# Optimization experiments

Measured on AMD Instinct MI355X. Metric: run time of the kernel, lower is better.

Reference implementation:

```python
import jax, jax.numpy as jnp
import numpy as np

N_NODES = 20000
N_EDGES = 320000
N_GRAPHS = 200
N_LAYERS = 2
TOWERS = 5
F_IN = 75        # divide_input=False -> each tower sees the full 75-dim input
F_OUT = 15       # out_channels // towers = 75 // 5
EDGE_DIM = 50
POST_IN = (4 * 3 + 1) * F_IN  # 4 aggregators * 3 scalers + self = 975
EPS_STD = 1e-5
EPS_BN = 1e-5


def setup_inputs() -> dict:
    key = jax.random.key(0)
    ks = jax.random.split(key, 16)
    x_idx = jax.random.randint(ks[0], (N_NODES,), 0, 10000)
    edge_index = jax.random.randint(ks[1], (2, N_EDGES), 0, N_NODES)
    edge_attr_idx = jax.random.randint(ks[2], (N_EDGES,), 0, 100)
    batch_idx = jnp.sort(jax.random.randint(ks[3], (N_NODES,), 0, N_GRAPHS))

    def g(k, shp, fan):
        return jax.random.normal(k, shp, jnp.float32) * np.float32(1.0 / np.sqrt(fan))

    inp = dict(
        x_idx=x_idx, edge_index=edge_index, edge_attr_idx=edge_attr_idx, batch_idx=batch_idx,
        node_emb=g(ks[4], (10000, F_IN), 1.0),
        edge_emb=g(ks[5], (100, EDGE_DIM), 1.0),
        W_edge=g(ks[6], (N_LAYERS, EDGE_DIM, F_IN), EDGE_DIM),
        b_edge=jnp.zeros((N_LAYERS, F_IN), jnp.float32),
        W_pre=g(ks[7], (N_LAYERS, TOWERS, 3 * F_IN, F_IN), 3 * F_IN),
        b_pre=jnp.zeros((N_LAYERS, TOWERS, F_IN), jnp.float32),
        W_post=g(ks[8], (N_LAYERS, TOWERS, POST_IN, F_OUT), POST_IN),
        b_post=jnp.zeros((N_LAYERS, TOWERS, F_OUT), jnp.float32),
        W_lin=g(ks[9], (N_LAYERS, F_IN, F_IN), F_IN),
        b_lin=jnp.zeros((N_LAYERS, F_IN), jnp.float32),
        bn_gamma=jnp.ones((N_LAYERS, F_IN), jnp.float32),
        bn_beta=jnp.zeros((N_LAYERS, F_IN), jnp.float32),
        W1=g(ks[10], (75, 50), 75), b1=jnp.zeros((50,), jnp.float32),
        W2=g(ks[11], (50, 25), 50), b2=jnp.zeros((25,), jnp.float32),
        W3=g(ks[12], (25, 1), 25), b3=jnp.zeros((1,), jnp.float32),
    )
    return inp


def reference(x_idx, edge_index, edge_attr_idx, batch_idx,
              node_emb, edge_emb, W_edge, b_edge, W_pre, b_pre,
              W_post, b_post, W_lin, b_lin, bn_gamma, bn_beta,
              W1, b1, W2, b2, W3, b3):
    src, dst = edge_index[0], edge_index[1]  # flow source_to_target: aggregate at dst
    x = node_emb[x_idx]                      # [N, 75]
    e_raw = edge_emb[edge_attr_idx]          # [E, 50]

    # in-degree based scalers (PNA); avg log-degree from this graph's degree histogram
    deg = jax.ops.segment_sum(jnp.ones((N_EDGES,), jnp.float32), dst, num_segments=N_NODES)
    avg_log = jnp.mean(jnp.log(deg + 1.0))
    deg_c = jnp.maximum(deg, 1.0)
    amp = (jnp.log(deg_c + 1.0) / avg_log)[:, None, None]
    att = (avg_log / jnp.log(deg_c + 1.0))[:, None, None]
    has_in = (deg > 0.0)[:, None, None]
    inv_deg = (1.0 / deg_c)[:, None, None]

    for l in range(N_LAYERS):
        # edge encoder (shared across towers)
        e = e_raw @ W_edge[l] + b_edge[l]                            # [E, 75]
        # message: since divide_input=False all towers see the same concat input
        h = jnp.concatenate([x[dst], x[src], e], axis=-1)            # [E, 225]
        m = jnp.einsum('ec,tcf->etf', h, W_pre[l]) + b_pre[l]        # [E, T, 75]
        # multi-aggregator reduction at dst
        mean = jax.ops.segment_sum(m, dst, num_segments=N_NODES) * inv_deg
        mean_sq = jax.ops.segment_sum(m * m, dst, num_segments=N_NODES) * inv_deg
        std = jnp.sqrt(jax.nn.relu(mean_sq - mean * mean) + EPS_STD)
        mn = jnp.where(has_in, jax.ops.segment_min(m, dst, num_segments=N_NODES), 0.0)
        mx = jnp.where(has_in, jax.ops.segment_max(m, dst, num_segments=N_NODES), 0.0)
        aggr = jnp.concatenate([mean, mn, mx, std], axis=-1)         # [N, T, 300]
        # degree scalers: identity, amplification, attenuation
        out = jnp.concatenate([aggr, aggr * amp, aggr * att], axis=-1)  # [N, T, 900]
        # update: concat self features, per-tower post MLP, then shared lin
        xt = jnp.broadcast_to(x[:, None, :], (N_NODES, TOWERS, F_IN))
        h2 = jnp.concatenate([xt, out], axis=-1)                     # [N, T, 975]
        y = jnp.einsum('ntc,tcf->ntf', h2, W_post[l]) + b_post[l]    # [N, T, 15]
        y = y.reshape(N_NODES, TOWERS * F_OUT) @ W_lin[l] + b_lin[l] # [N, 75]
        # BatchNorm (training-mode batch stats, biased variance) + ReLU
        mu = jnp.mean(y, axis=0)
        var = jnp.mean((y - mu) ** 2, axis=0)
        y = (y - mu) * jax.lax.rsqrt(var + EPS_BN) * bn_gamma[l] + bn_beta[l]
        x = jax.nn.relu(y)

    pooled = jax.ops.segment_sum(x, batch_idx, num_segments=N_GRAPHS)  # [G, 75]
    h = jax.nn.relu(pooled @ W1 + b1)
    h = jax.nn.relu(h @ W2 + b2)
    return h @ W3 + b3                                               # [G, 1]
```

## Files before the change

kernel.cpp:

```cpp
#include <hip/hip_runtime.h>
#include <hip/hip_bf16.h>
#include <math.h>

#define NN 20000
#define NE 320000
#define NG 200
#define FI 75
#define NT 5
#define FO 15
#define CH 375
#define PI 975

typedef __attribute__((ext_vector_type(8))) short v8s;
typedef __attribute__((ext_vector_type(4))) float v4f;

__device__ __forceinline__ unsigned short f2bfu(float v) {
  __hip_bfloat16 h = __float2bfloat16(v);
  return *reinterpret_cast<unsigned short*>(&h);
}
__device__ __forceinline__ float uif(unsigned u) { return __uint_as_float(u); }

__global__ __launch_bounds__(256) void k_mega1(
    const int* __restrict__ xidx, const float* __restrict__ emb, float* __restrict__ x,
    const int* __restrict__ dstp, int* __restrict__ deg,
    const float* __restrict__ eemb, const float* __restrict__ W_edge,
    const float* __restrict__ b_edge, float* __restrict__ te,
    const float* __restrict__ W_pre, float* __restrict__ WAs,
    const float* __restrict__ W_post, float* __restrict__ V,
    const float* __restrict__ b_post, const float* __restrict__ W_lin,
    const float* __restrict__ b_lin, float* __restrict__ bc) {
  __shared__ float S[FI * 16];
  int b = blockIdx.x, tid = threadIdx.x;
  if (b < 5860) {
    int i = b * 256 + tid;
    if (i < NN * FI) {
      int n = i / FI, f = i - n * FI;
      x[i] = emb[xidx[n] * FI + f];
    }
  } else if (b < 7110) {
    int e = (b - 5860) * 256 + tid;
    if (e < NE) atomicAdd(&deg[dstp[e]], 1);
  } else if (b < 7310) {
    int la = b - 7110;
    int l = la / 100, a = la - l * 100;
    int f = tid;
    if (f < FI) {
      float acc = b_edge[l * FI + f];
      for (int j = 0; j < 50; ++j)
        acc = fmaf(eemb[a * 50 + j], W_edge[(l * 50 + j) * FI + f], acc);
      te[la * FI + f] = acc;
    }
  } else if (b < 7530) {
    int i = (b - 7310) * 256 + tid;
    if (i < 2 * FI * CH) {
      int c = i % CH;
      int k = (i / CH) % FI;
      int l = i / (CH * FI);
      int t = c / FI, f = c - t * FI;
      WAs[i] = W_pre[((size_t)(l * NT + t) * 225 + FI + k) * FI + f];
    }
  } else if (b < 7560) {
    int bid = b - 7530;
    int g = bid % 3;
    int lt = bid / 3;
    for (int idx = tid; idx < FI * 16; idx += 256) {
      int q = idx >> 4, f = idx & 15;
      float v = 0.f;
      if (f < FO) {
        const float* wb = W_post + (size_t)lt * PI * FO;
        int rowb = FI + g * 300 + q;
        v = wb[rowb * FO + f] + wb[(rowb + FI) * FO + f] + wb[(rowb + 2 * FI) * FO + f];
      }
      S[idx] = v;
    }
    __syncthreads();
    for (int idx = tid; idx < FI * 16; idx += 256) {
      int j = idx >> 4, f = idx & 15;
      float acc = 0.f;
      const float* wr = W_pre + ((size_t)lt * 225 + j) * FI;
      for (int q = 0; q < FI; ++q) acc = fmaf(wr[q], S[q * 16 + f], acc);
      V[((size_t)bid * FI + j) * 16 + f] = acc;
    }
  } else {
    int l = b - 7560;
    int g = tid;
    if (g < FI) {
      float acc = b_lin[l * FI + g];
      for (int j = 0; j < FI; ++j)
        acc = fmaf(b_post[l * FI + j], W_lin[(l * FI + j) * FI + g], acc);
      bc[l * 76 + g] = acc;
    }
  }
}

__global__ __launch_bounds__(1024) void k_mega2(
    const int* __restrict__ deg, int* __restrict__ off, int* __restrict__ cur,
    float* __restrict__ avglog,
    const float* __restrict__ te, const float* __restrict__ W_pre,
    const float* __restrict__ b_pre, unsigned short* __restrict__ tm,
    const float* __restrict__ W_post, const float* __restrict__ V,
    unsigned short* __restrict__ Bp,
    const float* __restrict__ WAs, unsigned short* __restrict__ Bxs,
    const float* __restrict__ W_lin, unsigned short* __restrict__ Blin) {
  __shared__ float red[1024];
  int b = blockIdx.x, t = threadIdx.x;
  if (b == 0) {
    int* wsum = (int*)red;
    int base = t * 20;
    int loc[20];
    int s = 0;
#pragma unroll
    for (int j = 0; j < 20; ++j) {
      int i = base + j;
      int v = (i < NN) ? deg[i] : 0;
      loc[j] = s;
      s += v;
    }
    int lane = t & 63, w = t >> 6;
    int inc = s;
    for (int o = 1; o < 64; o <<= 1) {
      int u = __shfl_up(inc, o, 64);
      if (lane >= o) inc += u;
    }
    if (lane == 63) wsum[w] = inc;
    __syncthreads();
    if (t == 0) {
      int a = 0;
#pragma unroll
      for (int k = 0; k < 16; ++k) { int v = wsum[k]; wsum[k] = a; a += v; }
    }
    __syncthreads();
    int tex = wsum[w] + inc - s;
#pragma unroll
    for (int j = 0; j < 20; ++j) {
      int i = base + j;
      if (i < NN) { int e = tex + loc[j]; off[i] = e; cur[i] = e; }
    }
    if (t == 1023) off[NN] = tex + s;
  } else if (b == 1) {
    float s = 0.f;
    for (int i = t; i < NN; i += 1024) s += logf((float)deg[i] + 1.f);
    red[t] = s;
    __syncthreads();
    for (int o = 512; o > 0; o >>= 1) {
      if (t < o) red[t] += red[t + o];
      __syncthreads();
    }
    if (t == 0) avglog[0] = red[0] / (float)NN;
  } else if (b < 77) {
    int idx = (b - 2) * 1024 + t;
    if (idx < 76800) {
      int la = idx / 384, c = idx - la * 384;
      int l = la / 100;
      float acc = 0.f;
      if (c < CH) {
        int tt = c / FI, f = c - tt * FI;
        acc = b_pre[(l * NT + tt) * FI + f];
        const float* ter = te + la * FI;
        for (int k = 0; k < FI; ++k)
          acc = fmaf(ter[k], W_pre[((size_t)(l * NT + tt) * 225 + 150 + k) * FI + f], acc);
      }
      tm[(size_t)la * 384 + c] = f2bfu(acc);
    }
  } else if (b < 302) {
    int i = (b - 77) * 1024 + t;
    if (i < 230400) {
      int j = i & 7;
      int lane = (i >> 3) & 63;
      int rem = i >> 9;
      int kb = rem % 15; rem /= 15;
      int g = rem % 3; rem /= 3;
      int tt = rem % 5;
      int l = rem / 5;
      int k = kb * 32 + (lane >> 4) * 8 + j;
      int f = lane & 15;
      float w = 0.f;
      if (f < FO) {
        int lt = l * NT + tt;
        if (k < 300) {
          int a = k / 75, ch = k - a * 75;
          w = W_post[((size_t)lt * PI + FI + g * 300 + a * 75 + ch) * FO + f];
        } else if (k >= 320 && k < 395) {
          w = V[(((size_t)(lt * 3 + g)) * FI + (k - 320)) * 16 + f];
        } else if (k >= 395 && k < 470 && g == 0) {
          w = W_post[((size_t)lt * PI + (k - 395)) * FO + f];
        }
      }
      Bp[i] = f2bfu(w);
    }
  } else if (b < 374) {
    int i = (b - 302) * 1024 + t;
    if (i < 73728) {
      int j = i & 7;
      int lane = (i >> 3) & 63;
      int rem = i >> 9;
      int nt = rem % 24; rem /= 24;
      int kb = rem % 3;
      int l = rem / 3;
      int k = kb * 32 + (lane >> 4) * 8 + j;
      int n = nt * 16 + (lane & 15);
      float w = 0.f;
      if (k < FI && n < CH) w = WAs[(size_t)l * FI * CH + k * CH + n];
      Bxs[i] = f2bfu(w);
    }
  } else {
    int i = (b - 374) * 1024 + t;
    if (i < 15360) {
      int j = i & 7;
      int lane = (i >> 3) & 63;
      int rem = i >> 9;
      int nt = rem % 5; rem /= 5;
      int kb = rem % 3;
      int l = rem / 3;
      int k = kb * 32 + (lane >> 4) * 8 + j;
      int f = nt * 16 + (lane & 15);
      float w = 0.f;
      if (k < FI && f < FI) w = W_lin[(size_t)l * FI * FI + k * FI + f];
      Blin[i] = f2bfu(w);
    }
  }
}

__global__ __launch_bounds__(256) void k_mega3(
    const int* __restrict__ srcp, const int* __restrict__ dstp,
    const int* __restrict__ attr, int* __restrict__ cur, int2* __restrict__ csr,
    const int* __restrict__ deg, const float* __restrict__ avglog,
    float* __restrict__ amp, float* __restrict__ att, float* __restrict__ inv) {
  int b = blockIdx.x, t = threadIdx.x;
  if (b < 1250) {
    int e = b * 256 + t;
    if (e < NE) {
      int pos = atomicAdd(&cur[dstp[e]], 1);
      csr[pos] = make_int2(srcp[e], attr[e]);
    }
  } else {
    int i = (b - 1250) * 256 + t;
    if (i < NN) {
      float dc = fmaxf((float)deg[i], 1.f);
      float ld = logf(dc + 1.f);
      float av = avglog[0];
      amp[i] = ld / av;
      att[i] = av / ld;
      inv[i] = 1.f / dc;
    }
  }
}

__global__ __launch_bounds__(256) void k_gemm_xs(const float* __restrict__ x,
                                                 const unsigned short* __restrict__ BxsL,
                                                 unsigned short* __restrict__ xsb,
                                                 const int* __restrict__ deg,
                                                 unsigned short* __restrict__ xh,
                                                 float* __restrict__ bnsum) {
  int tid = threadIdx.x;
  if (blockIdx.y == 1) {
    if (blockIdx.x == 0 && tid < 150) bnsum[tid] = 0.f;
    for (int i = blockIdx.x * 256 + tid; i < NN * 160; i += 625 * 256) {
      int r = i / 160, k = i - r * 160;
      float v = 0.f;
      if (k < FI) v = x[(size_t)r * FI + k] * ((deg[r] > 0) ? 1.f : 0.f);
      else if (k < 150) v = x[(size_t)r * FI + k - FI];
      xh[i] = f2bfu(v);
    }
    return;
  }
  __shared__ unsigned short As[32 * 104];
  __shared__ unsigned short Os[32 * 384];
  int m0 = blockIdx.x * 32;
  for (int i = tid; i < 32 * 104; i += 256) {
    int r = i / 104, k = i - r * 104;
    As[i] = (k < FI) ? f2bfu(x[(size_t)(m0 + r) * FI + k]) : 0;
  }
  __syncthreads();
  int lane = tid & 63, w = tid >> 6;
  int m16 = lane & 15, quad = lane >> 4;
  v4f acc0[6], acc1[6];
#pragma unroll
  for (int nt = 0; nt < 6; ++nt) {
    acc0[nt] = {0.f, 0.f, 0.f, 0.f};
    acc1[nt] = {0.f, 0.f, 0.f, 0.f};
  }
  const unsigned short* arow0 = As + m16 * 104 + quad * 8;
  const unsigned short* arow1 = As + (16 + m16) * 104 + quad * 8;
#pragma unroll
  for (int kb = 0; kb < 3; ++kb) {
    v8s a0 = *(const v8s*)(arow0 + kb * 32);
    v8s a1 = *(const v8s*)(arow1 + kb * 32);
#pragma unroll
    for (int nt = 0; nt < 6; ++nt) {
      v8s bf = *(const v8s*)(BxsL + ((size_t)(kb * 24 + w * 6 + nt) * 64 + lane) * 8);
      acc0[nt] = __builtin_amdgcn_mfma_f32_16x16x32_bf16(a0, bf, acc0[nt], 0, 0, 0);
      acc1[nt] = __builtin_amdgcn_mfma_f32_16x16x32_bf16(a1, bf, acc1[nt], 0, 0, 0);
    }
  }
#pragma unroll
  for (int nt = 0; nt < 6; ++nt) {
    int col = w * 96 + nt * 16 + m16;
#pragma unroll
    for (int r = 0; r < 4; ++r) {
      Os[(quad * 4 + r) * 384 + col] = f2bfu(acc0[nt][r]);
      Os[(16 + quad * 4 + r) * 384 + col] = f2bfu(acc1[nt][r]);
    }
  }
  __syncthreads();
  uint4* dst = (uint4*)(xsb + (size_t)m0 * 384);
  const uint4* src = (const uint4*)Os;
  for (int i = tid; i < 1536; i += 256) dst[i] = src[i];
}

__global__ __launch_bounds__(192) void k_aggregate(int n0, int cn,
    const unsigned short* __restrict__ xs, const int2* __restrict__ csr,
    const int* __restrict__ off, const float* __restrict__ inv_deg,
    const unsigned short* __restrict__ tm, unsigned short* __restrict__ aggA) {
  __shared__ unsigned short sm[4 * 1600];
  int tid = threadIdx.x;
  int sub = tid / 48;
  int lane48 = tid - sub * 48;
  int rel0 = blockIdx.x * 4;
  int rel = rel0 + sub;
  for (int idx = tid; idx < 400; idx += 192) {
    int h = idx / 100, pp = idx - h * 100;
    int t = pp / 20, cc = pp - t * 20;
    sm[h * 1600 + t * 320 + 300 + cc] = 0;
  }
  if (rel < cn) {
    int n = n0 + rel;
    int c0 = lane48 * 8;
    int o0 = off[n], o1 = off[n + 1];
    float s[8], q[8], mn[8], mx[8];
#pragma unroll
    for (int j = 0; j < 8; ++j) {
      s[j] = 0.f; q[j] = 0.f; mn[j] = INFINITY; mx[j] = -INFINITY;
    }
    auto proc = [&](uint4 xv, uint4 tv) {
      unsigned xa[4] = {xv.x, xv.y, xv.z, xv.w};
      unsigned ta[4] = {tv.x, tv.y, tv.z, tv.w};
#pragma unroll
      for (int j = 0; j < 4; ++j) {
        float z0 = uif(xa[j] << 16) + uif(ta[j] << 16);
        float z1 = uif(xa[j] & 0xffff0000u) + uif(ta[j] & 0xffff0000u);
        s[2 * j] += z0; q[2 * j] = fmaf(z0, z0, q[2 * j]);
        mn[2 * j] = fminf(mn[2 * j], z0); mx[2 * j] = fmaxf(mx[2 * j], z0);
        s[2 * j + 1] += z1; q[2 * j + 1] = fmaf(z1, z1, q[2 * j + 1]);
        mn[2 * j + 1] = fminf(mn[2 * j + 1], z1); mx[2 * j + 1] = fmaxf(mx[2 * j + 1], z1);
      }
    };
    int i = o0;
    for (; i + 8 <= o1; i += 8) {
      int2 e0 = csr[i], e1 = csr[i + 1], e2 = csr[i + 2], e3 = csr[i + 3];
      int2 e4 = csr[i + 4], e5 = csr[i + 5], e6 = csr[i + 6], e7 = csr[i + 7];
      uint4 x0 = *(const uint4*)(xs + (size_t)e0.x * 384 + c0);
      uint4 t0 = *(const uint4*)(tm + (size_t)e0.y * 384 + c0);
      uint4 x1 = *(const uint4*)(xs + (size_t)e1.x * 384 + c0);
      uint4 t1 = *(const uint4*)(tm + (size_t)e1.y * 384 + c0);
      uint4 x2 = *(const uint4*)(xs + (size_t)e2.x * 384 + c0);
      uint4 t2 = *(const uint4*)(tm + (size_t)e2.y * 384 + c0);
      uint4 x3 = *(const uint4*)(xs + (size_t)e3.x * 384 + c0);
      uint4 t3 = *(const uint4*)(tm + (size_t)e3.y * 384 + c0);
      uint4 x4 = *(const uint4*)(xs + (size_t)e4.x * 384 + c0);
      uint4 t4 = *(const uint4*)(tm + (size_t)e4.y * 384 + c0);
      uint4 x5 = *(const uint4*)(xs + (size_t)e5.x * 384 + c0);
      uint4 t5 = *(const uint4*)(tm + (size_t)e5.y * 384 + c0);
      uint4 x6 = *(const uint4*)(xs + (size_t)e6.x * 384 + c0);
      uint4 t6 = *(const uint4*)(tm + (size_t)e6.y * 384 + c0);
      uint4 x7 = *(const uint4*)(xs + (size_t)e7.x * 384 + c0);
      uint4 t7 = *(const uint4*)(tm + (size_t)e7.y * 384 + c0);
      proc(x0, t0); proc(x1, t1); proc(x2, t2); proc(x3, t3);
      proc(x4, t4); proc(x5, t5); proc(x6, t6); proc(x7, t7);
    }
    for (; i + 2 <= o1; i += 2) {
      int2 e0 = csr[i], e1 = csr[i + 1];
      uint4 x0 = *(const uint4*)(xs + (size_t)e0.x * 384 + c0);
      uint4 t0 = *(const uint4*)(tm + (size_t)e0.y * 384 + c0);
      uint4 x1 = *(const uint4*)(xs + (size_t)e1.x * 384 + c0);
      uint4 t1 = *(const uint4*)(tm + (size_t)e1.y * 384 + c0);
      proc(x0, t0); proc(x1, t1);
    }
    if (i < o1) {
      int2 e0 = csr[i];
      uint4 x0 = *(const uint4*)(xs + (size_t)e0.x * 384 + c0);
      uint4 t0 = *(const uint4*)(tm + (size_t)e0.y * 384 + c0);
      proc(x0, t0);
    }
    float inv = inv_deg[n];
    bool empty = (o1 == o0);
    unsigned short* srow = sm + sub * 1600;
#pragma unroll
    for (int j = 0; j < 8; ++j) {
      int c = c0 + j;
      if (c < CH) {
        float me = s[j] * inv;
        float sd = sqrtf(fmaxf(q[j] * inv - me * me, 0.f) + 1e-5f);
        float mnv = empty ? 0.f : mn[j];
        float mxv = empty ? 0.f : mx[j];
        int t = c / 75, ch = c - t * 75;
        unsigned short* bb = srow + t * 320;
        bb[ch] = f2bfu(me);
        bb[75 + ch] = f2bfu(mnv);
        bb[150 + ch] = f2bfu(mxv);
        bb[225 + ch] = f2bfu(sd);
      }
    }
  }
  __syncthreads();
  int nrow = cn - rel0;
  if (nrow > 4) nrow = 4;
  if (nrow > 0) {
    int nu4 = nrow * 200;
    uint4* dst = (uint4*)(aggA + (size_t)rel0 * 1600);
    const uint4* src = (const uint4*)sm;
    for (int idx = tid; idx < nu4; idx += 192) dst[idx] = src[idx];
  }
}

__global__ __launch_bounds__(320) void k_post2(int n0, int nend,
    const unsigned short* __restrict__ aggA, const unsigned short* __restrict__ xh,
    const unsigned short* __restrict__ Bp, const float* __restrict__ amp,
    const float* __restrict__ att, const unsigned short* __restrict__ BlinL,
    const float* __restrict__ bcL, float* __restrict__ yout,
    float* __restrict__ bnsum) {
  __shared__ unsigned short zs[16 * 96];
  __shared__ float ysum[FI], ysq[FI];
  int tid = threadIdx.x;
  int lane = tid & 63, wv = tid >> 6;
  int m16 = lane & 15, quad = lane >> 4;
  if (tid < FI) { ysum[tid] = 0.f; ysq[tid] = 0.f; }
  for (int i = tid; i < 16 * 21; i += 320) {
    int r = i / 21, k = 75 + i - r * 21;
    zs[r * 96 + k] = 0;
  }
  int relA = blockIdx.x * 16 + m16;
  const unsigned short* arow = aggA + (size_t)relA * 1600 + wv * 320 + quad * 8;
  const unsigned short* xrow = xh + (size_t)(n0 + relA) * 160 + quad * 8;
  const unsigned short* bp = Bp + ((size_t)wv * 3 * 15 * 64) * 8 + lane * 8;
  v4f a0 = {0.f, 0.f, 0.f, 0.f}, a1 = a0, a2 = a0;
#pragma unroll
  for (int kb = 0; kb < 15; ++kb) {
    v8s av = *(const v8s*)((kb < 10) ? (arow + kb * 32) : (xrow + (kb - 10) * 32));
    const unsigned short* bb = bp + (size_t)kb * 512;
    v8s b0 = *(const v8s*)(bb);
    v8s b1 = *(const v8s*)(bb + 15 * 512);
    v8s b2 = *(const v8s*)(bb + 30 * 512);
    a0 = __builtin_amdgcn_mfma_f32_16x16x32_bf16(av, b0, a0, 0, 0, 0);
    a1 = __builtin_amdgcn_mfma_f32_16x16x32_bf16(av, b1, a1, 0, 0, 0);
    a2 = __builtin_amdgcn_mfma_f32_16x16x32_bf16(av, b2, a2, 0, 0, 0);
  }
  int f = m16;
  if (f < FO) {
    int relZ = quad * 4;
#pragma unroll
    for (int r = 0; r < 4; ++r) {
      int nd = n0 + blockIdx.x * 16 + relZ + r;
      int ndc = (nd < NN) ? nd : (NN - 1);
      float zz = a0[r] + amp[ndc] * a1[r] + att[ndc] * a2[r];
      zs[(relZ + r) * 96 + wv * FO + f] = f2bfu(zz);
    }
  }
  __syncthreads();
  const unsigned short* zrow = zs + m16 * 96 + quad * 8;
  v4f acc2 = {0.f, 0.f, 0.f, 0.f};
#pragma unroll
  for (int kb = 0; kb < 3; ++kb) {
    v8s av = *(const v8s*)(zrow + kb * 32);
    v8s bl = *(const v8s*)(BlinL + ((size_t)(kb * 5 + wv) * 64 + lane) * 8);
    acc2 = __builtin_amdgcn_mfma_f32_16x16x32_bf16(av, bl, acc2, 0, 0, 0);
  }
  int fcol = wv * 16 + m16;
  int nb = n0 + blockIdx.x * 16 + quad * 4;
  if (fcol < FI) {
    float bcf = bcL[fcol];
#pragma unroll
    for (int r = 0; r < 4; ++r) {
      int n = nb + r;
      if (n < nend) {
        float v = acc2[r] + bcf;
        yout[(size_t)n * FI + fcol] = v;
        atomicAdd(&ysum[fcol], v);
        atomicAdd(&ysq[fcol], v * v);
      }
    }
  }
  __syncthreads();
  if (tid < FI) {
    atomicAdd(&bnsum[tid], ysum[tid]);
    atomicAdd(&bnsum[FI + tid], ysq[tid]);
  }
}

__global__ __launch_bounds__(256) void k_bnfinapply(const float* __restrict__ y,
    const float* __restrict__ bnsum, const float* __restrict__ gamL,
    const float* __restrict__ betL, float* __restrict__ xo,
    const int* __restrict__ batch, float* __restrict__ pooled, int dopool) {
  __shared__ float sc[150];
  int tid = threadIdx.x;
  if (tid < FI) {
    float mu = bnsum[tid] / (float)NN;
    float var = bnsum[FI + tid] / (float)NN - mu * mu;
    float scl = gamL[tid] * rsqrtf(var + 1e-5f);
    sc[tid] = scl;
    sc[FI + tid] = betL[tid] - mu * scl;
  }
  if (!dopool) {
    for (int i = blockIdx.x * 256 + tid; i < NG * FI; i += gridDim.x * 256)
      pooled[i] = 0.f;
  }
  __syncthreads();
  int stride = gridDim.x * 256;
  for (int i = blockIdx.x * 256 + tid; i < NN * FI; i += stride) {
    int n = i / FI, f = i - n * FI;
    float v = fmaxf(fmaf(y[i], sc[f], sc[FI + f]), 0.f);
    xo[i] = v;
    if (dopool) atomicAdd(&pooled[batch[n] * FI + f], v);
  }
}

__global__ void k_head(const float* __restrict__ pooled, const float* __restrict__ W1,
                       const float* __restrict__ b1, const float* __restrict__ W2,
                       const float* __restrict__ b2, const float* __restrict__ W3,
                       const float* __restrict__ b3, float* __restrict__ out) {
  __shared__ float p[FI], h1[50], h2[25];
  int g = blockIdx.x, t = threadIdx.x;
  for (int i = t; i < FI; i += 64) p[i] = pooled[g * FI + i];
  __syncthreads();
  if (t < 50) {
    float a = b1[t];
    for (int j = 0; j < FI; ++j) a = fmaf(p[j], W1[j * 50 + t], a);
    h1[t] = fmaxf(a, 0.f);
  }
  __syncthreads();
  if (t < 25) {
    float a = b2[t];
    for (int j = 0; j < 50; ++j) a = fmaf(h1[j], W2[j * 25 + t], a);
    h2[t] = fmaxf(a, 0.f);
  }
  __syncthreads();
  if (t == 0) {
    float a = b3[0];
    for (int j = 0; j < 25; ++j) a = fmaf(h2[j], W3[j], a);
    out[g] = a;
  }
}

extern "C" void kernel_launch(void* const* d_in, const int* in_sizes, int n_in,
                              void* d_out, int out_size, void* d_ws, size_t ws_size,
                              hipStream_t stream) {
  const int* x_idx = (const int*)d_in[0];
  const int* eidx  = (const int*)d_in[1];
  const int* srcp  = eidx;
  const int* dstp  = eidx + NE;
  const int* eattr = (const int*)d_in[2];
  const int* batch = (const int*)d_in[3];
  const float* node_emb = (const float*)d_in[4];
  const float* edge_emb = (const float*)d_in[5];
  const float* W_edge = (const float*)d_in[6];
  const float* b_edge = (const float*)d_in[7];
  const float* W_pre  = (const float*)d_in[8];
  const float* b_pre  = (const float*)d_in[9];
  const float* W_post = (const float*)d_in[10];
  const float* b_post = (const float*)d_in[11];
  const float* W_lin  = (const float*)d_in[12];
  const float* b_lin  = (const float*)d_in[13];
  const float* gam = (const float*)d_in[14];
  const float* bet = (const float*)d_in[15];
  const float* W1 = (const float*)d_in[16];
  const float* b1 = (const float*)d_in[17];
  const float* W2 = (const float*)d_in[18];
  const float* b2 = (const float*)d_in[19];
  const float* W3 = (const float*)d_in[20];
  const float* b3 = (const float*)d_in[21];

  char* p = (char*)d_ws;
  auto alloc = [&](size_t b) -> char* {
    char* r = p;
    p += (b + 255) & ~(size_t)255;
    return r;
  };
  float* x_a   = (float*)alloc((size_t)NN * FI * 4);
  float* x_b   = (float*)alloc((size_t)NN * FI * 4);
  unsigned short* xs_bf = (unsigned short*)alloc((size_t)NN * 384 * 2);
  float* z     = (float*)alloc((size_t)NN * FI * 4);
  unsigned short* xh = (unsigned short*)alloc((size_t)(NN + 64) * 160 * 2);
  float* te    = (float*)alloc(2 * 100 * FI * 4);
  unsigned short* tm_bf = (unsigned short*)alloc((size_t)2 * 100 * 384 * 2);
  float* WAs   = (float*)alloc((size_t)2 * FI * CH * 4);
  float* V     = (float*)alloc((size_t)2 * NT * 3 * FI * 16 * 4);
  unsigned short* Bpk = (unsigned short*)alloc((size_t)230400 * 2);
  unsigned short* Bxs = (unsigned short*)alloc((size_t)73728 * 2);
  unsigned short* Blin = (unsigned short*)alloc((size_t)15360 * 2);
  float* bc    = (float*)alloc(2 * 76 * 4);
  float* ampv  = (float*)alloc((size_t)NN * 4);
  float* attv  = (float*)alloc((size_t)NN * 4);
  float* invv  = (float*)alloc((size_t)NN * 4);
  float* avglog = (float*)alloc(256);
  float* bnsum = (float*)alloc(2 * FI * 4);
  float* pooled = (float*)alloc((size_t)NG * FI * 4);
  int* deg = (int*)alloc((size_t)NN * 4);
  int* off = (int*)alloc((size_t)(NN + 1) * 4);
  int* cur = (int*)alloc((size_t)NN * 4);
  int2* csr = (int2*)alloc((size_t)NE * 8);
  size_t used = (size_t)(p - (char*)d_ws);
  int chunkN = NN;
  while (chunkN > 2500 &&
         used + (size_t)((chunkN + 63) & ~63) * 1600 * 2 + (1 << 20) > ws_size)
    chunkN >>= 1;
  int rows = (chunkN + 63) & ~63;
  unsigned short* aggA = (unsigned short*)alloc((size_t)rows * 1600 * 2);

  hipMemsetAsync(deg, 0, (size_t)NN * 4, stream);

  k_mega1<<<7562, 256, 0, stream>>>(x_idx, node_emb, x_a, dstp, deg,
                                    edge_emb, W_edge, b_edge, te,
                                    W_pre, WAs, W_post, V,
                                    b_post, W_lin, b_lin, bc);
  k_mega2<<<389, 1024, 0, stream>>>(deg, off, cur, avglog,
                                    te, W_pre, b_pre, tm_bf, W_post, V, Bpk,
                                    WAs, Bxs, W_lin, Blin);
  k_mega3<<<1329, 256, 0, stream>>>(srcp, dstp, eattr, cur, csr,
                                    deg, avglog, ampv, attv, invv);

  for (int l = 0; l < 2; ++l) {
    const float* xin = (l == 0) ? x_a : x_b;
    float* xout = (l == 0) ? x_b : x_a;
    k_gemm_xs<<<dim3(625, 2), 256, 0, stream>>>(xin, Bxs + (size_t)l * 36864,
                                                xs_bf, deg, xh, bnsum);
    for (int n0 = 0; n0 < NN; n0 += chunkN) {
      int cn = (NN - n0 < chunkN) ? (NN - n0) : chunkN;
      k_aggregate<<<(cn + 3) / 4, 192, 0, stream>>>(n0, cn, xs_bf, csr, off, invv,
                                                    tm_bf + (size_t)l * 100 * 384, aggA);
      k_post2<<<(cn + 15) / 16, 320, 0, stream>>>(
          n0, n0 + cn, aggA, xh, Bpk + (size_t)l * 115200, ampv, attv,
          Blin + (size_t)l * 7680, bc + l * 76, z, bnsum);
    }
    k_bnfinapply<<<1250, 256, 0, stream>>>(z, bnsum, gam + l * FI, bet + l * FI,
                                           xout, batch, pooled, (l == 1) ? 1 : 0);
  }

  k_head<<<NG, 64, 0, stream>>>(pooled, W1, b1, W2, b2, W3, b3, (float*)d_out);
}
```

Before: 476.2 us.

## Fuse neighbor aggregation and post-tower GEMM into one kernel via shared memory

Merges k_aggregate and k_post2 into a single 1024-thread kernel in which each of 16 waves aggregates one node into shared memory, then five waves run the tower MFMA GEMM and the lin GEMM directly from LDS. This removes the global aggA intermediate (about 64 MB written and read per layer) and the chunked launches. In exchange, the per-lane load width drops from 8 to 6 channels, the edge-loop unroll drops from 8 to 4, and 11 of 16 waves sit idle during the GEMM phase. The large LDS footprint also limits how many blocks fit per CU.

```diff
diff --git a/kernel.cpp b/kernel.cpp
--- a/kernel.cpp
+++ b/kernel.cpp
@@ -10,6 +10,7 @@
 #define FO 15
 #define CH 375
 #define PI 975
+#define SMS 1608
 
 typedef __attribute__((ext_vector_type(8))) short v8s;
 typedef __attribute__((ext_vector_type(4))) float v4f;
@@ -308,35 +309,44 @@
   for (int i = tid; i < 1536; i += 256) dst[i] = src[i];
 }
 
-__global__ __launch_bounds__(192) void k_aggregate(int n0, int cn,
+__global__ __launch_bounds__(1024) void k_aggpost(
     const unsigned short* __restrict__ xs, const int2* __restrict__ csr,
     const int* __restrict__ off, const float* __restrict__ inv_deg,
-    const unsigned short* __restrict__ tm, unsigned short* __restrict__ aggA) {
-  __shared__ unsigned short sm[4 * 1600];
+    const unsigned short* __restrict__ tm, const unsigned short* __restrict__ xh,
+    const unsigned short* __restrict__ Bp, const float* __restrict__ amp,
+    const float* __restrict__ att, const unsigned short* __restrict__ BlinL,
+    const float* __restrict__ bcL, float* __restrict__ yout,
+    float* __restrict__ bnsum) {
+  __shared__ __align__(16) unsigned short sm[16 * SMS];
+  __shared__ __align__(16) unsigned short zs[16 * 96];
+  __shared__ float ysum[FI], ysq[FI];
   int tid = threadIdx.x;
-  int sub = tid / 48;
-  int lane48 = tid - sub * 48;
-  int rel0 = blockIdx.x * 4;
-  int rel = rel0 + sub;
-  for (int idx = tid; idx < 400; idx += 192) {
+  int wv = tid >> 6, lane = tid & 63;
+  int rel0 = blockIdx.x * 16;
+  int n = rel0 + wv;
+  if (tid < FI) { ysum[tid] = 0.f; ysq[tid] = 0.f; }
+  for (int idx = tid; idx < 1600; idx += 1024) {
     int h = idx / 100, pp = idx - h * 100;
     int t = pp / 20, cc = pp - t * 20;
-    sm[h * 1600 + t * 320 + 300 + cc] = 0;
-  }
-  if (rel < cn) {
-    int n = n0 + rel;
-    int c0 = lane48 * 8;
+    sm[h * SMS + t * 320 + 300 + cc] = 0;
+  }
+  for (int i = tid; i < 16 * 21; i += 1024) {
+    int r = i / 21, k = 75 + i - r * 21;
+    zs[r * 96 + k] = 0;
+  }
+  if (n < NN) {
+    int c0 = lane * 6;
     int o0 = off[n], o1 = off[n + 1];
-    float s[8], q[8], mn[8], mx[8];
-#pragma unroll
-    for (int j = 0; j < 8; ++j) {
+    float s[6], q[6], mn[6], mx[6];
+#pragma unroll
+    for (int j = 0; j < 6; ++j) {
       s[j] = 0.f; q[j] = 0.f; mn[j] = INFINITY; mx[j] = -INFINITY;
     }
-    auto proc = [&](uint4 xv, uint4 tv) {
-      unsigned xa[4] = {xv.x, xv.y, xv.z, xv.w};
-      unsigned ta[4] = {tv.x, tv.y, tv.z, tv.w};
-#pragma unroll
-      for (int j = 0; j < 4; ++j) {
+    auto proc = [&](uint3 xv, uint3 tv) {
+      unsigned xa[3] = {xv.x, xv.y, xv.z};
+      unsigned ta[3] = {tv.x, tv.y, tv.z};
+#pragma unroll
+      for (int j = 0; j < 3; ++j) {
         float z0 = uif(xa[j] << 16) + uif(ta[j] << 16);
         float z1 = uif(xa[j] & 0xffff0000u) + uif(ta[j] & 0xffff0000u);
         s[2 * j] += z0; q[2 * j] = fmaf(z0, z0, q[2 * j]);
@@ -346,47 +356,29 @@
       }
     };
     int i = o0;
-    for (; i + 8 <= o1; i += 8) {
+    for (; i + 4 <= o1; i += 4) {
       int2 e0 = csr[i], e1 = csr[i + 1], e2 = csr[i + 2], e3 = csr[i + 3];
-      int2 e4 = csr[i + 4], e5 = csr[i + 5], e6 = csr[i + 6], e7 = csr[i + 7];
-      uint4 x0 = *(const uint4*)(xs + (size_t)e0.x * 384 + c0);
-      uint4 t0 = *(const uint4*)(tm + (size_t)e0.y * 384 + c0);
-      uint4 x1 = *(const uint4*)(xs + (size_t)e1.x * 384 + c0);
-      uint4 t1 = *(const uint4*)(tm + (size_t)e1.y * 384 + c0);
-      uint4 x2 = *(const uint4*)(xs + (size_t)e2.x * 384 + c0);
-      uint4 t2 = *(const uint4*)(tm + (size_t)e2.y * 384 + c0);
-      uint4 x3 = *(const uint4*)(xs + (size_t)e3.x * 384 + c0);
-      uint4 t3 = *(const uint4*)(tm + (size_t)e3.y * 384 + c0);
-      uint4 x4 = *(const uint4*)(xs + (size_t)e4.x * 384 + c0);
-      uint4 t4 = *(const uint4*)(tm + (size_t)e4.y * 384 + c0);
-      uint4 x5 = *(const uint4*)(xs + (size_t)e5.x * 384 + c0);
-      uint4 t5 = *(const uint4*)(tm + (size_t)e5.y * 384 + c0);
-      uint4 x6 = *(const uint4*)(xs + (size_t)e6.x * 384 + c0);
-      uint4 t6 = *(const uint4*)(tm + (size_t)e6.y * 384 + c0);
-      uint4 x7 = *(const uint4*)(xs + (size_t)e7.x * 384 + c0);
-      uint4 t7 = *(const uint4*)(tm + (size_t)e7.y * 384 + c0);
+      uint3 x0 = *(const uint3*)(xs + (size_t)e0.x * 384 + c0);
+      uint3 t0 = *(const uint3*)(tm + (size_t)e0.y * 384 + c0);
+      uint3 x1 = *(const uint3*)(xs + (size_t)e1.x * 384 + c0);
+      uint3 t1 = *(const uint3*)(tm + (size_t)e1.y * 384 + c0);
+      uint3 x2 = *(const uint3*)(xs + (size_t)e2.x * 384 + c0);
+      uint3 t2 = *(const uint3*)(tm + (size_t)e2.y * 384 + c0);
+      uint3 x3 = *(const uint3*)(xs + (size_t)e3.x * 384 + c0);
+      uint3 t3 = *(const uint3*)(tm + (size_t)e3.y * 384 + c0);
       proc(x0, t0); proc(x1, t1); proc(x2, t2); proc(x3, t3);
-      proc(x4, t4); proc(x5, t5); proc(x6, t6); proc(x7, t7);
-    }
-    for (; i + 2 <= o1; i += 2) {
-      int2 e0 = csr[i], e1 = csr[i + 1];
-      uint4 x0 = *(const uint4*)(xs + (size_t)e0.x * 384 + c0);
-      uint4 t0 = *(const uint4*)(tm + (size_t)e0.y * 384 + c0);
-      uint4 x1 = *(const uint4*)(xs + (size_t)e1.x * 384 + c0);
-      uint4 t1 = *(const uint4*)(tm + (size_t)e1.y * 384 + c0);
-      proc(x0, t0); proc(x1, t1);
-    }
-    if (i < o1) {
+    }
+    for (; i < o1; ++i) {
       int2 e0 = csr[i];
-      uint4 x0 = *(const uint4*)(xs + (size_t)e0.x * 384 + c0);
-      uint4 t0 = *(const uint4*)(tm + (size_t)e0.y * 384 + c0);
+      uint3 x0 = *(const uint3*)(xs + (size_t)e0.x * 384 + c0);
+      uint3 t0 = *(const uint3*)(tm + (size_t)e0.y * 384 + c0);
       proc(x0, t0);
     }
     float inv = inv_deg[n];
     bool empty = (o1 == o0);
-    unsigned short* srow = sm + sub * 1600;
-#pragma unroll
-    for (int j = 0; j < 8; ++j) {
+    unsigned short* srow = sm + wv * SMS;
+#pragma unroll
+    for (int j = 0; j < 6; ++j) {
       int c = c0 + j;
       if (c < CH) {
         float me = s[j] * inv;
@@ -401,82 +393,64 @@
         bb[225 + ch] = f2bfu(sd);
       }
     }
-  }
-  __syncthreads();
-  int nrow = cn - rel0;
-  if (nrow > 4) nrow = 4;
-  if (nrow > 0) {
-    int nu4 = nrow * 200;
-    uint4* dst = (uint4*)(aggA + (size_t)rel0 * 1600);
-    const uint4* src = (const uint4*)sm;
-    for (int idx = tid; idx < nu4; idx += 192) dst[idx] = src[idx];
-  }
-}
-
-__global__ __launch_bounds__(320) void k_post2(int n0, int nend,
-    const unsigned short* __restrict__ aggA, const unsigned short* __restrict__ xh,
-    const unsigned short* __restrict__ Bp, const float* __restrict__ amp,
-    const float* __restrict__ att, const unsigned short* __restrict__ BlinL,
-    const float* __restrict__ bcL, float* __restrict__ yout,
-    float* __restrict__ bnsum) {
-  __shared__ unsigned short zs[16 * 96];
-  __shared__ float ysum[FI], ysq[FI];
-  int tid = threadIdx.x;
-  int lane = tid & 63, wv = tid >> 6;
+  } else {
+    uint* rowz = (uint*)(sm + wv * SMS);
+    for (int idx2 = lane; idx2 < SMS / 2; idx2 += 64) rowz[idx2] = 0;
+  }
+  __syncthreads();
   int m16 = lane & 15, quad = lane >> 4;
-  if (tid < FI) { ysum[tid] = 0.f; ysq[tid] = 0.f; }
-  for (int i = tid; i < 16 * 21; i += 320) {
-    int r = i / 21, k = 75 + i - r * 21;
-    zs[r * 96 + k] = 0;
-  }
-  int relA = blockIdx.x * 16 + m16;
-  const unsigned short* arow = aggA + (size_t)relA * 1600 + wv * 320 + quad * 8;
-  const unsigned short* xrow = xh + (size_t)(n0 + relA) * 160 + quad * 8;
-  const unsigned short* bp = Bp + ((size_t)wv * 3 * 15 * 64) * 8 + lane * 8;
-  v4f a0 = {0.f, 0.f, 0.f, 0.f}, a1 = a0, a2 = a0;
-#pragma unroll
-  for (int kb = 0; kb < 15; ++kb) {
-    v8s av = *(const v8s*)((kb < 10) ? (arow + kb * 32) : (xrow + (kb - 10) * 32));
-    const unsigned short* bb = bp + (size_t)kb * 512;
-    v8s b0 = *(const v8s*)(bb);
-    v8s b1 = *(const v8s*)(bb + 15 * 512);
-    v8s b2 = *(const v8s*)(bb + 30 * 512);
-    a0 = __builtin_amdgcn_mfma_f32_16x16x32_bf16(av, b0, a0, 0, 0, 0);
-    a1 = __builtin_amdgcn_mfma_f32_16x16x32_bf16(av, b1, a1, 0, 0, 0);
-    a2 = __builtin_amdgcn_mfma_f32_16x16x32_bf16(av, b2, a2, 0, 0, 0);
-  }
-  int f = m16;
-  if (f < FO) {
-    int relZ = quad * 4;
-#pragma unroll
-    for (int r = 0; r < 4; ++r) {
-      int nd = n0 + blockIdx.x * 16 + relZ + r;
-      int ndc = (nd < NN) ? nd : (NN - 1);
-      float zz = a0[r] + amp[ndc] * a1[r] + att[ndc] * a2[r];
-      zs[(relZ + r) * 96 + wv * FO + f] = f2bfu(zz);
-    }
-  }
-  __syncthreads();
-  const unsigned short* zrow = zs + m16 * 96 + quad * 8;
-  v4f acc2 = {0.f, 0.f, 0.f, 0.f};
-#pragma unroll
-  for (int kb = 0; kb < 3; ++kb) {
-    v8s av = *(const v8s*)(zrow + kb * 32);
-    v8s bl = *(const v8s*)(BlinL + ((size_t)(kb * 5 + wv) * 64 + lane) * 8);
-    acc2 = __builtin_amdgcn_mfma_f32_16x16x32_bf16(av, bl, acc2, 0, 0, 0);
-  }
-  int fcol = wv * 16 + m16;
-  int nb = n0 + blockIdx.x * 16 + quad * 4;
-  if (fcol < FI) {
-    float bcf = bcL[fcol];
-#pragma unroll
-    for (int r = 0; r < 4; ++r) {
-      int n = nb + r;
-      if (n < nend) {
-        float v = acc2[r] + bcf;
-        yout[(size_t)n * FI + fcol] = v;
-        atomicAdd(&ysum[fcol], v);
-        atomicAdd(&ysq[fcol], v * v);
+  if (wv < NT) {
+    int tw = wv;
+    const unsigned short* arow = sm + m16 * SMS + tw * 320 + quad * 8;
+    const unsigned short* xrow = xh + (size_t)(rel0 + m16) * 160 + quad * 8;
+    const unsigned short* bp = Bp + ((size_t)tw * 3 * 15 * 64) * 8 + lane * 8;
+    v4f a0 = {0.f, 0.f, 0.f, 0.f}, a1 = a0, a2 = a0;
+#pragma unroll
+    for (int kb = 0; kb < 15; ++kb) {
+      v8s av = *(const v8s*)((kb < 10) ? (arow + kb * 32) : (xrow + (kb - 10) * 32));
+      const unsigned short* bb = bp + (size_t)kb * 512;
+      v8s b0 = *(const v8s*)(bb);
+      v8s b1 = *(const v8s*)(bb + 15 * 512);
+      v8s b2 = *(const v8s*)(bb + 30 * 512);
+      a0 = __builtin_amdgcn_mfma_f32_16x16x32_bf16(av, b0, a0, 0, 0, 0);
+      a1 = __builtin_amdgcn_mfma_f32_16x16x32_bf16(av, b1, a1, 0, 0, 0);
+      a2 = __builtin_amdgcn_mfma_f32_16x16x32_bf16(av, b2, a2, 0, 0, 0);
+    }
+    int f = m16;
+    if (f < FO) {
+      int relZ = quad * 4;
+#pragma unroll
+      for (int r = 0; r < 4; ++r) {
+        int nd = rel0 + relZ + r;
+        int ndc = (nd < NN) ? nd : (NN - 1);
+        float zz = a0[r] + amp[ndc] * a1[r] + att[ndc] * a2[r];
+        zs[(relZ + r) * 96 + tw * FO + f] = f2bfu(zz);
+      }
+    }
+  }
+  __syncthreads();
+  if (wv < NT) {
+    int tw = wv;
+    v4f acc2 = {0.f, 0.f, 0.f, 0.f};
+#pragma unroll
+    for (int kb = 0; kb < 3; ++kb) {
+      v8s av = *(const v8s*)(zs + m16 * 96 + quad * 8 + kb * 32);
+      v8s bl = *(const v8s*)(BlinL + ((size_t)(kb * 5 + tw) * 64 + lane) * 8);
+      acc2 = __builtin_amdgcn_mfma_f32_16x16x32_bf16(av, bl, acc2, 0, 0, 0);
+    }
+    int fcol = tw * 16 + m16;
+    if (fcol < FI) {
+      float bcf = bcL[fcol];
+      int nb = rel0 + quad * 4;
+#pragma unroll
+      for (int r = 0; r < 4; ++r) {
+        int nd = nb + r;
+        if (nd < NN) {
+          float v = acc2[r] + bcf;
+          yout[(size_t)nd * FI + fcol] = v;
+          atomicAdd(&ysum[fcol], v);
+          atomicAdd(&ysq[fcol], v * v);
+        }
       }
     }
   }
@@ -598,13 +572,6 @@
   int* off = (int*)alloc((size_t)(NN + 1) * 4);
   int* cur = (int*)alloc((size_t)NN * 4);
   int2* csr = (int2*)alloc((size_t)NE * 8);
-  size_t used = (size_t)(p - (char*)d_ws);
-  int chunkN = NN;
-  while (chunkN > 2500 &&
-         used + (size_t)((chunkN + 63) & ~63) * 1600 * 2 + (1 << 20) > ws_size)
-    chunkN >>= 1;
-  int rows = (chunkN + 63) & ~63;
-  unsigned short* aggA = (unsigned short*)alloc((size_t)rows * 1600 * 2);
 
   hipMemsetAsync(deg, 0, (size_t)NN * 4, stream);
 
@@ -623,14 +590,11 @@
     float* xout = (l == 0) ? x_b : x_a;
     k_gemm_xs<<<dim3(625, 2), 256, 0, stream>>>(xin, Bxs + (size_t)l * 36864,
                                                 xs_bf, deg, xh, bnsum);
-    for (int n0 = 0; n0 < NN; n0 += chunkN) {
-      int cn = (NN - n0 < chunkN) ? (NN - n0) : chunkN;
-      k_aggregate<<<(cn + 3) / 4, 192, 0, stream>>>(n0, cn, xs_bf, csr, off, invv,
-                                                    tm_bf + (size_t)l * 100 * 384, aggA);
-      k_post2<<<(cn + 15) / 16, 320, 0, stream>>>(
-          n0, n0 + cn, aggA, xh, Bpk + (size_t)l * 115200, ampv, attv,
-          Blin + (size_t)l * 7680, bc + l * 76, z, bnsum);
-    }
+    k_aggpost<<<1250, 1024, 0, stream>>>(xs_bf, csr, off, invv,
+                                         tm_bf + (size_t)l * 100 * 384, xh,
+                                         Bpk + (size_t)l * 115200, ampv, attv,
+                                         Blin + (size_t)l * 7680, bc + l * 76,
+                                         z, bnsum);
     k_bnfinapply<<<1250, 256, 0, stream>>>(z, bnsum, gam + l * FI, bet + l * FI,
                                            xout, batch, pooled, (l == 1) ? 1 : 0);
   }
```

Result: faster. 432.3 us (-9.2%).
